# Performance work log

Hardware: AMD Instinct MI355X
Metric: run time of the kernel (lower is better)

## Reference

```python
import jax, jax.numpy as jnp
import numpy as np

B, S, WIN, E, H, L = 32, 1024, 1024, 128, 512, 3


def setup_inputs() -> dict:
    key = jax.random.key(0)
    ks = jax.random.split(key, 12)
    rn = lambda k, shape: jax.random.normal(k, shape, dtype=jnp.float32) * 0.05
    z = lambda *shape: jnp.zeros(shape, dtype=jnp.float32)
    return {
        "inputs": jax.random.normal(ks[0], (B, S, WIN), dtype=jnp.float32),
        "mask": jnp.ones((B, S, 1), dtype=jnp.float32),
        "lengths": jnp.full((B,), S, dtype=jnp.int32),  # full-length sequences
        "W_e": rn(ks[1], (E, WIN)), "b_e": z(E),
        "W_a1": rn(ks[2], (E, E)), "b_a1": z(E),
        "W_a2": rn(ks[3], (L, E)), "b_a2": z(L),
        "Wih_e": rn(ks[4], (4 * H, E)), "Whh_e": rn(ks[5], (4 * H, H)),
        "bih_e": z(4 * H), "bhh_e": z(4 * H),
        "enc_h0": z(H), "enc_c0": z(H),
        "Wih_d": rn(ks[6], (4 * H, 1 + H)), "Whh_d": rn(ks[7], (4 * H, H)),
        "bih_d": z(4 * H), "bhh_d": z(4 * H),
        "dec_h0": z(H), "dec_c0": z(H),
        "W_o1": rn(ks[8], (E, H)), "b_o1": z(E),
        "W_o2": rn(ks[9], (1, E)), "b_o2": z(1),
    }


def _cell(gates, c):
    # PyTorch LSTM gate order: i, f, g, o
    i, f, g, o = jnp.split(gates, 4, axis=-1)
    c = jax.nn.sigmoid(f) * c + jax.nn.sigmoid(i) * jnp.tanh(g)
    h = jax.nn.sigmoid(o) * jnp.tanh(c)
    return h, c


def reference(inputs, mask, lengths,
              W_e, b_e, W_a1, b_a1, W_a2, b_a2,
              Wih_e, Whh_e, bih_e, bhh_e, enc_h0, enc_c0,
              Wih_d, Whh_d, bih_d, bhh_d, dec_h0, dec_c0,
              W_o1, b_o1, W_o2, b_o2):
    # embed MLP (dropout inactive at eval)
    embed = jax.nn.relu(jnp.einsum('bsw,ew->bse', inputs, W_e) + b_e)  # (B,S,E)
    # local-attention weights; nn.Softmax(dim=1) normalizes over TIME (faithful)
    a = jax.nn.relu(embed @ W_a1.T + b_a1) @ W_a2.T + b_a2              # (B,S,L)
    attn = jax.nn.softmax(a, axis=1)

    # ---- encoder LSTM (single layer, learned h0/c0) ----
    x_proj = jnp.einsum('bse,ge->bsg', embed, Wih_e) + (bih_e + bhh_e)  # (B,S,4H)
    h0 = jnp.broadcast_to(enc_h0, (B, H))
    c0 = jnp.broadcast_to(enc_c0, (B, H))

    def enc_step(carry, xp):
        h, c = carry
        h, c = _cell(xp + h @ Whh_e.T, c)
        return (h, c), h

    _, enc_hs = jax.lax.scan(enc_step, (h0, c0), jnp.swapaxes(x_proj, 0, 1))
    enc_out = jnp.swapaxes(enc_hs, 0, 1)                                # (B,S,H)
    # pad_packed_sequence zeros positions past each length
    t_idx = jnp.arange(S)[None, :, None]
    enc_out = jnp.where(t_idx < lengths[:, None, None], enc_out, 0.0)

    # ---- convolve: context[b,t] = sum_i attn[b,t,i] * enc_out[b,t-i] ----
    context = attn[..., 0:1] * enc_out
    for i in range(1, L):  # L=3, tiny fixed loop
        shifted = jnp.pad(enc_out[:, :-i, :], ((0, 0), (i, 0), (0, 0)))
        context = context + attn[..., i:i + 1] * shifted

    dh0 = jnp.broadcast_to(dec_h0, (B, H))
    dc0 = jnp.broadcast_to(dec_c0, (B, H))
    p0 = jnp.zeros((B, 1), dtype=inputs.dtype)  # tgt_init = 0.0
    b_d = bih_d + bhh_d

    def dec_step(carry, ctx_t):
        h, c, p = carry
        x = jnp.concatenate([p, ctx_t], axis=1)                         # (B,1+H)
        h, c = _cell(x @ Wih_d.T + h @ Whh_d.T + b_d, c)
        p = jax.nn.relu(h @ W_o1.T + b_o1) @ W_o2.T + b_o2              # (B,1)
        return (h, c, p), p

    _, ps = jax.lax.scan(dec_step, (dh0, dc0, p0), jnp.swapaxes(context, 0, 1))
    predicted = jnp.swapaxes(ps, 0, 1)                                  # (B,S,1)
    return predicted * mask
```

## Files before the change

### kernel.cpp

```cpp
#include <hip/hip_runtime.h>
#include <cstddef>

__device__ __forceinline__ float sigm(float x) { return 1.f / (1.f + __expf(-x)); }
__device__ __forceinline__ float tanh_(float x) { return 1.f - 2.f / (__expf(2.f * x) + 1.f); }

#define AGLD(p)    __hip_atomic_load((p),  __ATOMIC_RELAXED, __HIP_MEMORY_SCOPE_AGENT)
#define AGST(p, v) __hip_atomic_store((p), (v), __ATOMIC_RELAXED, __HIP_MEMORY_SCOPE_AGENT)
#define AGADD(p,v) __hip_atomic_fetch_add((p), (v), __ATOMIC_RELAXED, __HIP_MEMORY_SCOPE_AGENT)

#define DOT16(wp, hp, kk) do { \
    float4 w0_ = *(const float4*)((wp) + (kk));      float4 x0_ = *(const float4*)((hp) + (kk)); \
    float4 w1_ = *(const float4*)((wp) + (kk) + 4);  float4 x1_ = *(const float4*)((hp) + (kk) + 4); \
    float4 w2_ = *(const float4*)((wp) + (kk) + 8);  float4 x2_ = *(const float4*)((hp) + (kk) + 8); \
    float4 w3_ = *(const float4*)((wp) + (kk) + 12); float4 x3_ = *(const float4*)((hp) + (kk) + 12); \
    a0 = fmaf(w0_.x, x0_.x, a0); a0 = fmaf(w0_.y, x0_.y, a0); a0 = fmaf(w0_.z, x0_.z, a0); a0 = fmaf(w0_.w, x0_.w, a0); \
    a1 = fmaf(w1_.x, x1_.x, a1); a1 = fmaf(w1_.y, x1_.y, a1); a1 = fmaf(w1_.z, x1_.z, a1); a1 = fmaf(w1_.w, x1_.w, a1); \
    a2 = fmaf(w2_.x, x2_.x, a2); a2 = fmaf(w2_.y, x2_.y, a2); a2 = fmaf(w2_.z, x2_.z, a2); a2 = fmaf(w2_.w, x2_.w, a2); \
    a3 = fmaf(w3_.x, x3_.x, a3); a3 = fmaf(w3_.y, x3_.y, a3); a3 = fmaf(w3_.z, x3_.z, a3); a3 = fmaf(w3_.w, x3_.w, a3); \
  } while (0)

__global__ __launch_bounds__(256) void k_embed(
    const float* __restrict__ inp, const float* __restrict__ We,
    const float* __restrict__ be, float* __restrict__ emb)
{
  __shared__ float sA[32 * 68];
  __shared__ float sW[32 * 132];
  const int tid = threadIdx.x;
  const int b  = blockIdx.x >> 4;
  const int s0 = (blockIdx.x & 15) << 6;
  float acc[4][8];
#pragma unroll
  for (int i = 0; i < 4; ++i)
#pragma unroll
    for (int j = 0; j < 8; ++j) acc[i][j] = 0.f;
  const int m4 = (tid & 15) << 2;
  const int e8 = (tid >> 4) << 3;
  const float* Ab = inp + ((size_t)(b << 10) + s0) * 1024;
  const int ms = tid >> 2, kq = tid & 3;
  const int es = tid >> 1, kq2 = tid & 1;
  for (int k0 = 0; k0 < 1024; k0 += 32) {
    __syncthreads();
    {
      const float* src = Ab + (size_t)ms * 1024 + k0 + (kq << 3);
      float4 v0 = *(const float4*)(src);
      float4 v1 = *(const float4*)(src + 4);
      int kb = kq << 3;
      sA[(kb+0)*68+ms] = v0.x; sA[(kb+1)*68+ms] = v0.y;
      sA[(kb+2)*68+ms] = v0.z; sA[(kb+3)*68+ms] = v0.w;
      sA[(kb+4)*68+ms] = v1.x; sA[(kb+5)*68+ms] = v1.y;
      sA[(kb+6)*68+ms] = v1.z; sA[(kb+7)*68+ms] = v1.w;
    }
    {
      const float* src = We + (size_t)es * 1024 + k0 + (kq2 << 4);
#pragma unroll
      for (int q = 0; q < 4; ++q) {
        float4 v = *(const float4*)(src + (q << 2));
        int kb = (kq2 << 4) + (q << 2);
        sW[(kb+0)*132+es] = v.x; sW[(kb+1)*132+es] = v.y;
        sW[(kb+2)*132+es] = v.z; sW[(kb+3)*132+es] = v.w;
      }
    }
    __syncthreads();
#pragma unroll 4
    for (int kk = 0; kk < 32; ++kk) {
      float4 a4 = *(const float4*)&sA[kk*68 + m4];
      float4 b0 = *(const float4*)&sW[kk*132 + e8];
      float4 b1 = *(const float4*)&sW[kk*132 + e8 + 4];
      float av[4] = {a4.x, a4.y, a4.z, a4.w};
      float bv[8] = {b0.x, b0.y, b0.z, b0.w, b1.x, b1.y, b1.z, b1.w};
#pragma unroll
      for (int i = 0; i < 4; ++i)
#pragma unroll
        for (int j = 0; j < 8; ++j) acc[i][j] = fmaf(av[i], bv[j], acc[i][j]);
    }
  }
#pragma unroll
  for (int i = 0; i < 4; ++i) {
    int s = s0 + m4 + i;
#pragma unroll
    for (int j = 0; j < 8; ++j) {
      float v = acc[i][j] + be[e8 + j];
      emb[((size_t)(s << 5) + b) * 128 + e8 + j] = v > 0.f ? v : 0.f;
    }
  }
}

__global__ __launch_bounds__(256) void k_attn(
    const float* __restrict__ emb, const float* __restrict__ Wa1,
    const float* __restrict__ ba1, const float* __restrict__ Wa2,
    const float* __restrict__ ba2, float* __restrict__ aw)
{
  __shared__ float sE[2 * 128];
  __shared__ float sH[2 * 128];
  const int tid = threadIdx.x;
  const int rs0 = blockIdx.x * 2;
  sE[tid] = emb[(size_t)rs0 * 128 + tid];
  __syncthreads();
  const int half = tid >> 7, j = tid & 127;
  const float* w = Wa1 + j * 128;
  const float* e = sE + half * 128;
  float a0 = 0.f, a1 = 0.f, a2 = 0.f, a3 = 0.f;
  for (int k = 0; k < 128; k += 16) DOT16(w, e, k);
  float h = (a0 + a1) + (a2 + a3) + ba1[j];
  sH[half * 128 + j] = h > 0.f ? h : 0.f;
  __syncthreads();
  if (tid < 6) {
    int hh = tid / 3, l = tid % 3;
    const float* w2 = Wa2 + l * 128;
    const float* hv = sH + hh * 128;
    float s = 0.f;
    for (int k = 0; k < 128; ++k) s = fmaf(w2[k], hv[k], s);
    aw[(size_t)(rs0 + hh) * 3 + l] = s + ba2[l];
  }
}

__global__ __launch_bounds__(256) void k_softmax(float* __restrict__ aw)
{
  __shared__ float red[256];
  const int b = blockIdx.x / 3, l = blockIdx.x % 3;
  const int tid = threadIdx.x;
  float v[4];
#pragma unroll
  for (int i = 0; i < 4; ++i) {
    int s = tid + i * 256;
    v[i] = aw[(size_t)(s * 32 + b) * 3 + l];
  }
  float mx = fmaxf(fmaxf(v[0], v[1]), fmaxf(v[2], v[3]));
  red[tid] = mx;
  __syncthreads();
  for (int off = 128; off > 0; off >>= 1) {
    if (tid < off) red[tid] = fmaxf(red[tid], red[tid + off]);
    __syncthreads();
  }
  mx = red[0];
  __syncthreads();
  float sm = 0.f;
#pragma unroll
  for (int i = 0; i < 4; ++i) sm += __expf(v[i] - mx);
  red[tid] = sm;
  __syncthreads();
  for (int off = 128; off > 0; off >>= 1) {
    if (tid < off) red[tid] += red[tid + off];
    __syncthreads();
  }
  float inv = 1.f / red[0];
#pragma unroll
  for (int i = 0; i < 4; ++i) {
    int s = tid + i * 256;
    aw[(size_t)(s * 32 + b) * 3 + l] = __expf(v[i] - mx) * inv;
  }
}

__global__ __launch_bounds__(256) void k_prep(
    const float* __restrict__ Wih_d,
    const float* __restrict__ bih_e, const float* __restrict__ bhh_e,
    const float* __restrict__ bih_d, const float* __restrict__ bhh_d,
    float* __restrict__ wdpack, float* __restrict__ bsum_e, float* __restrict__ bsum_d)
{
  const int row = blockIdx.x;
  const int tid = threadIdx.x;
  for (int q = tid; q < 516; q += 256) {
    float v = 0.f;
    if (q < 512)      v = Wih_d[(size_t)row * 513 + 1 + q];
    else if (q == 512) v = Wih_d[(size_t)row * 513];
    wdpack[(size_t)row * 516 + q] = v;
  }
  if (tid == 0) {
    bsum_e[row] = bih_e[row] + bhh_e[row];
    bsum_d[row] = bih_d[row] + bhh_d[row];
  }
}

__global__ __launch_bounds__(256) void k_init(
    const float* __restrict__ eh0, const float* __restrict__ dh0,
    const float* __restrict__ bo2,
    float* __restrict__ heb, float* __restrict__ hdb,
    float* __restrict__ out, unsigned* __restrict__ bar)
{
  const int i = blockIdx.x * 256 + threadIdx.x;
  if (i < 16384) {
    int k = i & 511;
    heb[16384 + i] = eh0[k];
    hdb[i] = dh0[k];
  }
  out[i] = bo2[0];
  if (i < 1024) bar[i] = 0u;
}

__device__ __forceinline__ void groupbar(unsigned* gbar, int r, unsigned gen)
{
  __builtin_amdgcn_s_waitcnt(0);
  __syncthreads();
  if (threadIdx.x == 0) {
    asm volatile("" ::: "memory");
    unsigned old = AGADD(gbar + ((r >> 3) << 4), 1u);
    if (old == (gen << 3) - 1u)
      (void)AGADD(gbar + 128, 1u);
    while (AGLD(gbar + 128) < (gen << 3))
      __builtin_amdgcn_s_sleep(1);
    asm volatile("" ::: "memory");
  }
  __syncthreads();
}

#define OUT_DUTY(TI) do { \
    const int e_ = (r << 3) + (tid >> 5); \
    const int ob_ = (tid >> 2) & 7; \
    const int kq_ = tid & 3; \
    const float* wo_ = Wo1 + (size_t)e_ * 512 + (kq_ << 7); \
    const float* hd_ = sHd + ob_ * 516 + (kq_ << 7); \
    float a0 = 0.f, a1 = 0.f, a2 = 0.f, a3 = 0.f; \
    _Pragma("unroll") \
    for (int k = 0; k < 128; k += 16) DOT16(wo_, hd_, k); \
    float p_ = (a0 + a1) + (a2 + a3); \
    p_ += __shfl_down(p_, 1); \
    p_ += __shfl_down(p_, 2); \
    float contrib_ = 0.f; \
    if (kq_ == 0) { \
      float q_ = p_ + bo1[e_]; \
      contrib_ = (q_ > 0.f ? q_ : 0.f) * Wo2[e_]; \
    } \
    contrib_ += __shfl_down(contrib_, 32); \
    { \
      const int lane_ = tid & 63, wv_ = tid >> 6; \
      if (lane_ < 32 && (lane_ & 3) == 0) sRed[(wv_ << 3) + (lane_ >> 2)] = contrib_; \
    } \
    __syncthreads(); \
    if (tid < 8) \
      atomicAdd(&out[(size_t)(gb8 + tid) * 1024 + (TI)], \
                sRed[tid] + sRed[8 + tid] + sRed[16 + tid] + sRed[24 + tid]); \
  } while (0)

__global__ __launch_bounds__(256) void k_persist(
    const float* __restrict__ emb, const float* __restrict__ aw,
    const int* __restrict__ lens,
    const float* __restrict__ Wih_e, const float* __restrict__ Whh_e,
    const float* __restrict__ Whh_d, const float* __restrict__ wdpack,
    const float* __restrict__ bsum_e, const float* __restrict__ bsum_d,
    const float* __restrict__ ec0, const float* __restrict__ dc0,
    const float* __restrict__ Wo1, const float* __restrict__ bo1,
    const float* __restrict__ Wo2, const float* __restrict__ maskp,
    float* __restrict__ heb, float* __restrict__ hdb,
    float* __restrict__ ctxb, float* __restrict__ out,
    unsigned* __restrict__ bar)
{
  __shared__ float sX[8 * 516];
  __shared__ float sHd[8 * 516];
  __shared__ float sEmb[8 * 132];
  __shared__ float sG[256];
  __shared__ float sP[8];
  __shared__ float sRed[32];

  const int tid = threadIdx.x;
  const int g = blockIdx.x >> 6;
  const int r = blockIdx.x & 63;
  const int rr = tid >> 3;
  const int bb = tid & 7;
  const int grow = ((rr >> 3) << 9) + (r << 3) + (rr & 7);
  const int gb8 = g << 3;

  unsigned* gbar = bar + g * 160;

  const float be_row = bsum_e[grow];
  const float bd_row = bsum_d[grow];
  const float pcoef  = wdpack[(size_t)grow * 516 + 512];

  float c_e = 0.f, c_d = 0.f, hm1 = 0.f, hm2 = 0.f;
  int len_b = 0;
  if (tid < 64) {
    int dim = (r << 3) + (tid >> 3);
    c_e = ec0[dim];
    c_d = dc0[dim];
    len_b = lens[gb8 + (tid & 7)];
  }

  const float* whe = Whh_e + (size_t)grow * 512;
  const float* wie = Wih_e + (size_t)grow * 128;
  const float* whd = Whh_d + (size_t)grow * 512;
  const float* wdc = wdpack + (size_t)grow * 516;
  const float* hX  = sX   + bb * 516;
  const float* hD  = sHd  + bb * 516;
  const float* hE  = sEmb + bb * 132;

  unsigned gen = 0;

  for (int t = 0; t < 1024; ++t) {
    {
      const float* hep = heb + (size_t)((t + 1) & 1) * 16384 + (size_t)gb8 * 512;
      const float* hdp = hdb + (size_t)gb8 * 512;
      float vHe[16], vHd[16];
#pragma unroll
      for (int j = 0; j < 16; ++j) {
        vHe[j] = AGLD(hep + tid + j * 256);
        vHd[j] = AGLD(hdp + tid + j * 256);
      }
      float4 ev = *(const float4*)(emb + (size_t)(t * 32 + gb8 + (tid >> 5)) * 128 + ((tid & 31) << 2));
#pragma unroll
      for (int j = 0; j < 16; ++j) {
        int i = tid + j * 256, bi = i >> 9, kk = i & 511;
        sX [bi * 516 + kk] = vHe[j];
        sHd[bi * 516 + kk] = vHd[j];
      }
      *(float4*)(sEmb + (tid >> 5) * 132 + ((tid & 31) << 2)) = ev;
    }
    __syncthreads();

    {
      float a0 = 0.f, a1 = 0.f, a2 = 0.f, a3 = 0.f;
#pragma unroll 4
      for (int k = 0; k < 512; k += 16) DOT16(whe, hX, k);
#pragma unroll
      for (int k = 0; k < 128; k += 16) DOT16(wie, hE, k);
      sG[(rr << 3) + bb] = (a0 + a1) + (a2 + a3) + be_row;
    }

    if (r < 16 && t > 0) { OUT_DUTY(t - 1); }

    __syncthreads();

    if (tid < 64) {
      float gi = sG[tid], gf = sG[64 + tid], gg = sG[128 + tid], go = sG[192 + tid];
      c_e = sigm(gf) * c_e + sigm(gi) * tanh_(gg);
      float h = sigm(go) * tanh_(c_e);
      int dim = (r << 3) + (tid >> 3);
      int gb = gb8 + (tid & 7);
      AGST(&heb[(size_t)(t & 1) * 16384 + (size_t)gb * 512 + dim], h);
      float hmv = (t < len_b) ? h : 0.f;
      const float* at = aw + (size_t)(t * 32 + gb) * 3;
      float ctx = at[0] * hmv + at[1] * hm1 + at[2] * hm2;
      hm2 = hm1; hm1 = hmv;
      AGST(&ctxb[(size_t)gb * 512 + dim], ctx);
    }
    groupbar(gbar, r, ++gen);

    {
      const float* cp = ctxb + (size_t)gb8 * 512;
      float vC[16];
#pragma unroll
      for (int j = 0; j < 16; ++j) vC[j] = AGLD(cp + tid + j * 256);
#pragma unroll
      for (int j = 0; j < 16; ++j) {
        int i = tid + j * 256, bi = i >> 9, kk = i & 511;
        sX[bi * 516 + kk] = vC[j];
      }
      if (tid < 8) sP[tid] = (t == 0) ? 0.f : AGLD(&out[(size_t)(gb8 + tid) * 1024 + (t - 1)]);
    }
    __syncthreads();

    {
      float a0 = 0.f, a1 = 0.f, a2 = 0.f, a3 = 0.f;
#pragma unroll 2
      for (int k = 0; k < 512; k += 16) { DOT16(whd, hD, k); DOT16(wdc, hX, k); }
      sG[(rr << 3) + bb] = (a0 + a1) + (a2 + a3) + pcoef * sP[bb] + bd_row;
    }
    __syncthreads();

    if (tid < 64) {
      float gi = sG[tid], gf = sG[64 + tid], gg = sG[128 + tid], go = sG[192 + tid];
      c_d = sigm(gf) * c_d + sigm(gi) * tanh_(gg);
      float h = sigm(go) * tanh_(c_d);
      int dim = (r << 3) + (tid >> 3);
      AGST(&hdb[(size_t)(gb8 + (tid & 7)) * 512 + dim], h);
    }
    groupbar(gbar, r, ++gen);
  }

  if (r < 16) {
    const float* hdp = hdb + (size_t)gb8 * 512;
    float vHd[16];
#pragma unroll
    for (int j = 0; j < 16; ++j) vHd[j] = AGLD(hdp + tid + j * 256);
#pragma unroll
    for (int j = 0; j < 16; ++j) {
      int i = tid + j * 256, bi = i >> 9, kk = i & 511;
      sHd[bi * 516 + kk] = vHd[j];
    }
    __syncthreads();
    OUT_DUTY(1023);
  }
  groupbar(gbar, r, ++gen);

  if (tid < 128) {
    int idx = blockIdx.x * 128 + tid;
    float v = AGLD(&out[idx]);
    out[idx] = v * maskp[idx];
  }
}

extern "C" void kernel_launch(void* const* d_in, const int* in_sizes, int n_in,
                              void* d_out, int out_size, void* d_ws, size_t ws_size,
                              hipStream_t stream)
{
  const float* inp   = (const float*)d_in[0];
  const float* maskp = (const float*)d_in[1];
  const int*   lens  = (const int*)d_in[2];
  const float* We    = (const float*)d_in[3];
  const float* be    = (const float*)d_in[4];
  const float* Wa1   = (const float*)d_in[5];
  const float* ba1   = (const float*)d_in[6];
  const float* Wa2   = (const float*)d_in[7];
  const float* ba2   = (const float*)d_in[8];
  const float* Wih_e = (const float*)d_in[9];
  const float* Whh_e = (const float*)d_in[10];
  const float* bih_e = (const float*)d_in[11];
  const float* bhh_e = (const float*)d_in[12];
  const float* eh0   = (const float*)d_in[13];
  const float* ec0   = (const float*)d_in[14];
  const float* Wih_d = (const float*)d_in[15];
  const float* Whh_d = (const float*)d_in[16];
  const float* bih_d = (const float*)d_in[17];
  const float* bhh_d = (const float*)d_in[18];
  const float* dh0   = (const float*)d_in[19];
  const float* dc0   = (const float*)d_in[20];
  const float* Wo1   = (const float*)d_in[21];
  const float* bo1   = (const float*)d_in[22];
  const float* Wo2   = (const float*)d_in[23];
  const float* bo2   = (const float*)d_in[24];

  float* ws     = (float*)d_ws;
  float* emb    = ws;
  float* aw     = emb + 4194304;
  float* heb    = aw + 98304;
  float* hdb    = heb + 32768;
  float* ctxb   = hdb + 16384;
  float* wdpack = ctxb + 16384;
  float* bsum_e = wdpack + 1056768;
  float* bsum_d = bsum_e + 2048;
  unsigned* bar = (unsigned*)(bsum_d + 2048);
  float* outf = (float*)d_out;

  k_embed<<<512, 256, 0, stream>>>(inp, We, be, emb);
  k_attn<<<16384, 256, 0, stream>>>(emb, Wa1, ba1, Wa2, ba2, aw);
  k_softmax<<<96, 256, 0, stream>>>(aw);
  k_prep<<<2048, 256, 0, stream>>>(Wih_d, bih_e, bhh_e, bih_d, bhh_d,
                                   wdpack, bsum_e, bsum_d);
  k_init<<<128, 256, 0, stream>>>(eh0, dh0, bo2, heb, hdb, outf, bar);

  k_persist<<<256, 256, 0, stream>>>(
      emb, aw, lens,
      Wih_e, Whh_e, Whh_d, wdpack, bsum_e, bsum_d,
      ec0, dc0, Wo1, bo1, Wo2, maskp,
      heb, hdb, ctxb, outf, bar);
}
```

Measured before the change: 28.56 ms.

## Skew encoder and decoder steps into one pipelined loop with single barrier

Restructures the persistent kernel so that encoder step i, decoder step i-1 and the output MLP for step i-2 run in the same iteration. This halves the number of group-wide barriers per time step, from two to one. Hidden-state and context buffers become double-buffered. The output projection moves to 8 blocks that each compute a full prediction and publish it through a per-batch flag that decoder threads spin on. In exchange it adds a point-to-point flag wait on the decoder's critical path and a longer serial output computation per block, with some risk of stalls or memory-ordering problems.

```diff
diff --git a/kernel.cpp b/kernel.cpp
--- a/kernel.cpp
+++ b/kernel.cpp
@@ -181,7 +181,7 @@
   if (i < 16384) {
     int k = i & 511;
     heb[16384 + i] = eh0[k];
-    hdb[i] = dh0[k];
+    hdb[16384 + i] = dh0[k];
   }
   out[i] = bo2[0];
   if (i < 1024) bar[i] = 0u;
@@ -203,34 +203,6 @@
   __syncthreads();
 }
 
-#define OUT_DUTY(TI) do { \
-    const int e_ = (r << 3) + (tid >> 5); \
-    const int ob_ = (tid >> 2) & 7; \
-    const int kq_ = tid & 3; \
-    const float* wo_ = Wo1 + (size_t)e_ * 512 + (kq_ << 7); \
-    const float* hd_ = sHd + ob_ * 516 + (kq_ << 7); \
-    float a0 = 0.f, a1 = 0.f, a2 = 0.f, a3 = 0.f; \
-    _Pragma("unroll") \
-    for (int k = 0; k < 128; k += 16) DOT16(wo_, hd_, k); \
-    float p_ = (a0 + a1) + (a2 + a3); \
-    p_ += __shfl_down(p_, 1); \
-    p_ += __shfl_down(p_, 2); \
-    float contrib_ = 0.f; \
-    if (kq_ == 0) { \
-      float q_ = p_ + bo1[e_]; \
-      contrib_ = (q_ > 0.f ? q_ : 0.f) * Wo2[e_]; \
-    } \
-    contrib_ += __shfl_down(contrib_, 32); \
-    { \
-      const int lane_ = tid & 63, wv_ = tid >> 6; \
-      if (lane_ < 32 && (lane_ & 3) == 0) sRed[(wv_ << 3) + (lane_ >> 2)] = contrib_; \
-    } \
-    __syncthreads(); \
-    if (tid < 8) \
-      atomicAdd(&out[(size_t)(gb8 + tid) * 1024 + (TI)], \
-                sRed[tid] + sRed[8 + tid] + sRed[16 + tid] + sRed[24 + tid]); \
-  } while (0)
-
 __global__ __launch_bounds__(256) void k_persist(
     const float* __restrict__ emb, const float* __restrict__ aw,
     const int* __restrict__ lens,
@@ -239,17 +211,18 @@
     const float* __restrict__ bsum_e, const float* __restrict__ bsum_d,
     const float* __restrict__ ec0, const float* __restrict__ dc0,
     const float* __restrict__ Wo1, const float* __restrict__ bo1,
-    const float* __restrict__ Wo2, const float* __restrict__ maskp,
+    const float* __restrict__ Wo2, const float* __restrict__ bo2,
+    const float* __restrict__ maskp,
     float* __restrict__ heb, float* __restrict__ hdb,
     float* __restrict__ ctxb, float* __restrict__ out,
     unsigned* __restrict__ bar)
 {
-  __shared__ float sX[8 * 516];
+  __shared__ float sHe[8 * 516];
+  __shared__ float sCtx[8 * 516];
   __shared__ float sHd[8 * 516];
   __shared__ float sEmb[8 * 132];
-  __shared__ float sG[256];
-  __shared__ float sP[8];
-  __shared__ float sRed[32];
+  __shared__ float sGe[256], sGd[256];
+  __shared__ float sRed[4];
 
   const int tid = threadIdx.x;
   const int g = blockIdx.x >> 6;
@@ -259,126 +232,150 @@
   const int grow = ((rr >> 3) << 9) + (r << 3) + (rr & 7);
   const int gb8 = g << 3;
 
-  unsigned* gbar = bar + g * 160;
+  unsigned* gbar  = bar + g * 160;
+  unsigned* pflag = bar + 768;
 
   const float be_row = bsum_e[grow];
   const float bd_row = bsum_d[grow];
-  const float pcoef  = wdpack[(size_t)grow * 516 + 512];
+  const float bo2v = bo2[0];
 
   float c_e = 0.f, c_d = 0.f, hm1 = 0.f, hm2 = 0.f;
+  float pc0 = 0.f, pc1 = 0.f, pc2 = 0.f, pc3 = 0.f;
   int len_b = 0;
   if (tid < 64) {
     int dim = (r << 3) + (tid >> 3);
     c_e = ec0[dim];
     c_d = dc0[dim];
     len_b = lens[gb8 + (tid & 7)];
+    pc0 = wdpack[(size_t)(0 * 512 + dim) * 516 + 512];
+    pc1 = wdpack[(size_t)(1 * 512 + dim) * 516 + 512];
+    pc2 = wdpack[(size_t)(2 * 512 + dim) * 516 + 512];
+    pc3 = wdpack[(size_t)(3 * 512 + dim) * 516 + 512];
   }
 
   const float* whe = Whh_e + (size_t)grow * 512;
   const float* wie = Wih_e + (size_t)grow * 128;
   const float* whd = Whh_d + (size_t)grow * 512;
   const float* wdc = wdpack + (size_t)grow * 516;
-  const float* hX  = sX   + bb * 516;
+  const float* hX  = sHe  + bb * 516;
+  const float* hC  = sCtx + bb * 516;
   const float* hD  = sHd  + bb * 516;
   const float* hE  = sEmb + bb * 132;
 
-  unsigned gen = 0;
-
-  for (int t = 0; t < 1024; ++t) {
+  for (int i = 0; i < 1026; ++i) {
+    const bool doEnc = (i < 1024);
+    const bool doDec = (i >= 1) && (i < 1025);
+    const bool doOut = (i >= 2);
+
     {
-      const float* hep = heb + (size_t)((t + 1) & 1) * 16384 + (size_t)gb8 * 512;
-      const float* hdp = hdb + (size_t)gb8 * 512;
-      float vHe[16], vHd[16];
+      const float* hep = heb  + (size_t)((i + 1) & 1) * 16384 + (size_t)gb8 * 512;
+      const float* cpp = ctxb + (size_t)((i + 1) & 1) * 16384 + (size_t)gb8 * 512;
+      const float* hdp = hdb  + (size_t)(i & 1) * 16384 + (size_t)gb8 * 512;
+      float vHe[16], vC[16], vHd[16];
 #pragma unroll
       for (int j = 0; j < 16; ++j) {
         vHe[j] = AGLD(hep + tid + j * 256);
+        vC[j]  = AGLD(cpp + tid + j * 256);
         vHd[j] = AGLD(hdp + tid + j * 256);
       }
-      float4 ev = *(const float4*)(emb + (size_t)(t * 32 + gb8 + (tid >> 5)) * 128 + ((tid & 31) << 2));
+      float4 ev = {0.f, 0.f, 0.f, 0.f};
+      if (doEnc)
+        ev = *(const float4*)(emb + (size_t)(i * 32 + gb8 + (tid >> 5)) * 128 + ((tid & 31) << 2));
 #pragma unroll
       for (int j = 0; j < 16; ++j) {
-        int i = tid + j * 256, bi = i >> 9, kk = i & 511;
-        sX [bi * 516 + kk] = vHe[j];
-        sHd[bi * 516 + kk] = vHd[j];
-      }
-      *(float4*)(sEmb + (tid >> 5) * 132 + ((tid & 31) << 2)) = ev;
-    }
-    __syncthreads();
-
-    {
+        int ii = tid + j * 256, bi = ii >> 9, kk = ii & 511;
+        sHe [bi * 516 + kk] = vHe[j];
+        sCtx[bi * 516 + kk] = vC[j];
+        sHd [bi * 516 + kk] = vHd[j];
+      }
+      if (doEnc)
+        *(float4*)(sEmb + (tid >> 5) * 132 + ((tid & 31) << 2)) = ev;
+    }
+    __syncthreads();
+
+    if (r < 8 && doOut) {
+      const int ob = gb8 + r;
+      const int e2 = tid << 1;
+      const float* w0 = Wo1 + (size_t)e2 * 512;
+      const float* hd = sHd + r * 516;
+      float a0 = 0.f, a1 = 0.f, a2 = 0.f, a3 = 0.f;
+#pragma unroll 4
+      for (int k = 0; k < 512; k += 8) {
+        float4 x0 = *(const float4*)(hd + k), x1 = *(const float4*)(hd + k + 4);
+        float4 u0 = *(const float4*)(w0 + k), u1 = *(const float4*)(w0 + k + 4);
+        float4 q0 = *(const float4*)(w0 + 512 + k), q1 = *(const float4*)(w0 + 512 + k + 4);
+        a0 = fmaf(u0.x,x0.x,a0); a0 = fmaf(u0.y,x0.y,a0); a0 = fmaf(u0.z,x0.z,a0); a0 = fmaf(u0.w,x0.w,a0);
+        a1 = fmaf(u1.x,x1.x,a1); a1 = fmaf(u1.y,x1.y,a1); a1 = fmaf(u1.z,x1.z,a1); a1 = fmaf(u1.w,x1.w,a1);
+        a2 = fmaf(q0.x,x0.x,a2); a2 = fmaf(q0.y,x0.y,a2); a2 = fmaf(q0.z,x0.z,a2); a2 = fmaf(q0.w,x0.w,a2);
+        a3 = fmaf(q1.x,x1.x,a3); a3 = fmaf(q1.y,x1.y,a3); a3 = fmaf(q1.z,x1.z,a3); a3 = fmaf(q1.w,x1.w,a3);
+      }
+      float d0 = (a0 + a1) + bo1[e2];
+      float d1 = (a2 + a3) + bo1[e2 + 1];
+      float contrib = (d0 > 0.f ? d0 : 0.f) * Wo2[e2] + (d1 > 0.f ? d1 : 0.f) * Wo2[e2 + 1];
+      contrib += __shfl_down(contrib, 32);
+      contrib += __shfl_down(contrib, 16);
+      contrib += __shfl_down(contrib, 8);
+      contrib += __shfl_down(contrib, 4);
+      contrib += __shfl_down(contrib, 2);
+      contrib += __shfl_down(contrib, 1);
+      if ((tid & 63) == 0) sRed[tid >> 6] = contrib;
+      __syncthreads();
+      if (tid == 0) {
+        float p = sRed[0] + sRed[1] + sRed[2] + sRed[3] + bo2v;
+        AGST(&out[(size_t)ob * 1024 + (i - 2)], p);
+        __builtin_amdgcn_s_waitcnt(0);
+        AGST(&pflag[ob << 3], (unsigned)i);
+      }
+    }
+
+    if (doEnc) {
       float a0 = 0.f, a1 = 0.f, a2 = 0.f, a3 = 0.f;
 #pragma unroll 4
       for (int k = 0; k < 512; k += 16) DOT16(whe, hX, k);
 #pragma unroll
       for (int k = 0; k < 128; k += 16) DOT16(wie, hE, k);
-      sG[(rr << 3) + bb] = (a0 + a1) + (a2 + a3) + be_row;
-    }
-
-    if (r < 16 && t > 0) { OUT_DUTY(t - 1); }
-
-    __syncthreads();
-
-    if (tid < 64) {
-      float gi = sG[tid], gf = sG[64 + tid], gg = sG[128 + tid], go = sG[192 + tid];
-      c_e = sigm(gf) * c_e + sigm(gi) * tanh_(gg);
-      float h = sigm(go) * tanh_(c_e);
-      int dim = (r << 3) + (tid >> 3);
-      int gb = gb8 + (tid & 7);
-      AGST(&heb[(size_t)(t & 1) * 16384 + (size_t)gb * 512 + dim], h);
-      float hmv = (t < len_b) ? h : 0.f;
-      const float* at = aw + (size_t)(t * 32 + gb) * 3;
-      float ctx = at[0] * hmv + at[1] * hm1 + at[2] * hm2;
-      hm2 = hm1; hm1 = hmv;
-      AGST(&ctxb[(size_t)gb * 512 + dim], ctx);
-    }
-    groupbar(gbar, r, ++gen);
-
-    {
-      const float* cp = ctxb + (size_t)gb8 * 512;
-      float vC[16];
-#pragma unroll
-      for (int j = 0; j < 16; ++j) vC[j] = AGLD(cp + tid + j * 256);
-#pragma unroll
-      for (int j = 0; j < 16; ++j) {
-        int i = tid + j * 256, bi = i >> 9, kk = i & 511;
-        sX[bi * 516 + kk] = vC[j];
-      }
-      if (tid < 8) sP[tid] = (t == 0) ? 0.f : AGLD(&out[(size_t)(gb8 + tid) * 1024 + (t - 1)]);
-    }
-    __syncthreads();
-
-    {
+      sGe[(rr << 3) + bb] = (a0 + a1) + (a2 + a3) + be_row;
+    }
+    if (doDec) {
       float a0 = 0.f, a1 = 0.f, a2 = 0.f, a3 = 0.f;
 #pragma unroll 2
-      for (int k = 0; k < 512; k += 16) { DOT16(whd, hD, k); DOT16(wdc, hX, k); }
-      sG[(rr << 3) + bb] = (a0 + a1) + (a2 + a3) + pcoef * sP[bb] + bd_row;
+      for (int k = 0; k < 512; k += 16) { DOT16(whd, hD, k); DOT16(wdc, hC, k); }
+      sGd[(rr << 3) + bb] = (a0 + a1) + (a2 + a3) + bd_row;
     }
     __syncthreads();
 
     if (tid < 64) {
-      float gi = sG[tid], gf = sG[64 + tid], gg = sG[128 + tid], go = sG[192 + tid];
-      c_d = sigm(gf) * c_d + sigm(gi) * tanh_(gg);
-      float h = sigm(go) * tanh_(c_d);
-      int dim = (r << 3) + (tid >> 3);
-      AGST(&hdb[(size_t)(gb8 + (tid & 7)) * 512 + dim], h);
-    }
-    groupbar(gbar, r, ++gen);
-  }
-
-  if (r < 16) {
-    const float* hdp = hdb + (size_t)gb8 * 512;
-    float vHd[16];
-#pragma unroll
-    for (int j = 0; j < 16; ++j) vHd[j] = AGLD(hdp + tid + j * 256);
-#pragma unroll
-    for (int j = 0; j < 16; ++j) {
-      int i = tid + j * 256, bi = i >> 9, kk = i & 511;
-      sHd[bi * 516 + kk] = vHd[j];
-    }
-    __syncthreads();
-    OUT_DUTY(1023);
-  }
-  groupbar(gbar, r, ++gen);
+      const int dim = (r << 3) + (tid >> 3);
+      const int gb = gb8 + (tid & 7);
+      if (doEnc) {
+        float gi = sGe[tid], gf = sGe[64 + tid], gg = sGe[128 + tid], go = sGe[192 + tid];
+        c_e = sigm(gf) * c_e + sigm(gi) * tanh_(gg);
+        float h = sigm(go) * tanh_(c_e);
+        AGST(&heb[(size_t)(i & 1) * 16384 + (size_t)gb * 512 + dim], h);
+        float hmv = (i < len_b) ? h : 0.f;
+        const float* at = aw + (size_t)(i * 32 + gb) * 3;
+        float ctx = at[0] * hmv + at[1] * hm1 + at[2] * hm2;
+        hm2 = hm1; hm1 = hmv;
+        AGST(&ctxb[(size_t)(i & 1) * 16384 + (size_t)gb * 512 + dim], ctx);
+      }
+      if (doDec) {
+        float p = 0.f;
+        if (doOut) {
+          unsigned* fl = &pflag[gb << 3];
+          while (AGLD(fl) < (unsigned)i) __builtin_amdgcn_s_sleep(1);
+          p = AGLD(&out[(size_t)gb * 1024 + (i - 2)]);
+        }
+        float gi = sGd[tid]       + pc0 * p;
+        float gf = sGd[64 + tid]  + pc1 * p;
+        float gg = sGd[128 + tid] + pc2 * p;
+        float go = sGd[192 + tid] + pc3 * p;
+        c_d = sigm(gf) * c_d + sigm(gi) * tanh_(gg);
+        float h = sigm(go) * tanh_(c_d);
+        AGST(&hdb[(size_t)((i + 1) & 1) * 16384 + (size_t)gb * 512 + dim], h);
+      }
+    }
+    groupbar(gbar, r, (unsigned)(i + 1));
+  }
 
   if (tid < 128) {
     int idx = blockIdx.x * 128 + tid;
@@ -422,8 +419,8 @@
   float* aw     = emb + 4194304;
   float* heb    = aw + 98304;
   float* hdb    = heb + 32768;
-  float* ctxb   = hdb + 16384;
-  float* wdpack = ctxb + 16384;
+  float* ctxb   = hdb + 32768;
+  float* wdpack = ctxb + 32768;
   float* bsum_e = wdpack + 1056768;
   float* bsum_d = bsum_e + 2048;
   unsigned* bar = (unsigned*)(bsum_d + 2048);
@@ -439,6 +436,6 @@
   k_persist<<<256, 256, 0, stream>>>(
       emb, aw, lens,
       Wih_e, Whh_e, Whh_d, wdpack, bsum_e, bsum_d,
-      ec0, dc0, Wo1, bo1, Wo2, maskp,
+      ec0, dc0, Wo1, bo1, Wo2, bo2, maskp,
       heb, hdb, ctxb, outf, bar);
 }
```

Result: slower. 53.61 ms (+87.7%).
